# Kernel optimization log

Hardware: AMD Instinct MI355X
Metric: run time of the kernel (lower is better)

Reference implementation:

```python
import jax, jax.numpy as jnp
import numpy as np


def setup_inputs() -> dict:
    key = jax.random.key(0)
    k1, k2, k3 = jax.random.split(key, 3)
    preds = jax.random.normal(k1, (8, 3, 2048, 8), dtype=jnp.float32)
    gts = jax.random.normal(k2, (8, 3, 2048), dtype=jnp.float32)
    idx = jax.random.randint(k3, (64, 2), 0, 8, dtype=jnp.int64)
    return {"preds": preds, "gts": gts, "idx": idx}


def reference(preds, gts, idx):
    # preds: [bs, 3, N, seeds], gts: [bs, 3, N], idx: [num, 2] (batch, seed)
    num = idx.shape[0]
    # select (batch, seed) pairs -> [num, 3, N]
    p = jnp.transpose(preds, (0, 3, 1, 2))[idx[:, 0], idx[:, 1]]
    # gts expanded over seeds is constant in seed -> just index batch
    g = gts[idx[:, 0]]  # [num, 3, N]
    x = jnp.transpose(p, (0, 2, 1))  # [num, N, 3]
    y = jnp.transpose(g, (0, 2, 1))  # [num, N, 3]
    # P[b, i, j] = ||x_i||^2 + ||y_j||^2 - 2 x_i . y_j
    rx = jnp.sum(x * x, axis=-1)  # [num, N]
    ry = jnp.sum(y * y, axis=-1)  # [num, N]
    zz = jnp.einsum('bid,bjd->bij', x, y)  # [num, N, N]
    P = rx[:, :, None] + ry[:, None, :] - 2.0 * zz
    loss_1 = jnp.sum(jnp.min(P, axis=1))  # min over x for each y
    loss_2 = jnp.sum(jnp.min(P, axis=2))  # min over y for each x
    return (loss_1 + loss_2) / num
```

## Files before the change

### kernel.cpp

```cpp
#include <hip/hip_runtime.h>


#define NPTS 2048
#define NB 64
#define BLK 256

#define PREDS_A 49152
#define PREDS_C 16384
#define GTS_A 6144
#define GTS_C 2048

#define OFF_ROW   0
#define OFF_CPART 524288
#define OFF_PART  8912896
#define OFF_QPK   8916992
#define OFF_YPK   13111296
#define WS_REQ    17305600

using bf16x8  = __attribute__((ext_vector_type(8))) __bf16;
using short8v = __attribute__((ext_vector_type(8))) short;
using f32x16  = __attribute__((ext_vector_type(16))) float;

static __device__ __forceinline__ unsigned short f2bf(float f) {
    unsigned u = __float_as_uint(f);
    u = u + 0x7FFFu + ((u >> 16) & 1u);
    return (unsigned short)(u >> 16);
}
static __device__ __forceinline__ float bf2f(unsigned short h) {
    return __uint_as_float(((unsigned)h) << 16);
}
static __device__ __forceinline__ float min3f(float a, float b, float c) {
    return fminf(fminf(a, b), c);
}
static __device__ __forceinline__ float ctree(f32x16 a) {
    const float c0 = min3f(a[0], a[1], a[2]);
    const float c1 = min3f(a[3], a[4], a[5]);
    const float c2 = min3f(a[6], a[7], a[8]);
    const float c3 = min3f(a[9], a[10], a[11]);
    const float c4 = min3f(a[12], a[13], a[14]);
    const float d0 = min3f(c0, c1, a[15]);
    const float d1 = min3f(c2, c3, c4);
    return fminf(d0, d1);
}

__global__ __launch_bounds__(256) void cf_pack2(
    const float* __restrict__ preds, const float* __restrict__ gts,
    const int* __restrict__ idx,
    unsigned short* __restrict__ qpk, unsigned short* __restrict__ ypk)
{
    const int blk = blockIdx.x, tid = threadIdx.x;
    const unsigned short one = 0x3F80;
    if (blk < 512) {
        const int p = blk * 256 + tid;
        const int b = p >> 11, i = p & 2047;
        const int i0 = idx[2 * b], m1 = idx[2 * b + 1];
        const float* pb = preds + i0 * PREDS_A + m1 + i * 8;
        const float x0 = pb[0], x1 = pb[PREDS_C], x2 = pb[2 * PREDS_C];
        const float rx = fmaf(x0, x0, fmaf(x1, x1, x2 * x2));
        const float a0 = -2.f * x0, a1 = -2.f * x1, a2 = -2.f * x2;
        const unsigned short h0 = f2bf(a0), h1 = f2bf(a1), h2 = f2bf(a2);
        const unsigned short l0 = f2bf(a0 - bf2f(h0));
        const unsigned short l1 = f2bf(a1 - bf2f(h1));
        const unsigned short l2 = f2bf(a2 - bf2f(h2));
        const unsigned short rh = f2bf(rx), rl = f2bf(rx - bf2f(rh));
        alignas(16) unsigned short t[16] =
            {h0, h1, h2, h0, h1, h2, l0, l1, l2, rh, rl, one, one, 0, 0, 0};
        uint4* dst = (uint4*)(qpk + (size_t)p * 16);
        dst[0] = *(const uint4*)&t[0];
        dst[1] = *(const uint4*)&t[8];
    } else {
        const int p = (blk - 512) * 256 + tid;
        const int b = p >> 11, j = p & 2047;
        const int i0 = idx[2 * b];
        const float* gb = gts + i0 * GTS_A + j;
        const float y0 = gb[0], y1 = gb[GTS_C], y2 = gb[2 * GTS_C];
        const float ry = fmaf(y0, y0, fmaf(y1, y1, y2 * y2));
        const unsigned short h0 = f2bf(y0), h1 = f2bf(y1), h2 = f2bf(y2);
        const unsigned short l0 = f2bf(y0 - bf2f(h0));
        const unsigned short l1 = f2bf(y1 - bf2f(h1));
        const unsigned short l2 = f2bf(y2 - bf2f(h2));
        const unsigned short rh = f2bf(ry), rl = f2bf(ry - bf2f(rh));
        alignas(16) unsigned short t[16] =
            {h0, h1, h2, l0, l1, l2, h0, h1, h2, one, one, rh, rl, 0, 0, 0};
        uint4* dst = (uint4*)(ypk + (size_t)p * 16);
        dst[0] = *(const uint4*)&t[0];
        dst[1] = *(const uint4*)&t[8];
    }
}

__global__ __launch_bounds__(BLK, 4) void cf_mf3c(
    const unsigned short* __restrict__ qpk, const unsigned short* __restrict__ ypk,
    float* __restrict__ rowbuf, float* __restrict__ colpart)
{
    const int tid = threadIdx.x;
    const int bid = blockIdx.x;
    const int strip = bid & 15;
    const int b = bid >> 4;

    __shared__ float scolw[4][NPTS];

    const int l = tid & 63, w = tid >> 6;
    const int lc = l & 31, lh = l >> 5;

    const short8v* qv = (const short8v*)qpk;
    const short8v* yv = (const short8v*)ypk;

    const int arow = b * NPTS + strip * 128 + w * 32 + lc;
    const bf16x8 afrag = __builtin_bit_cast(bf16x8, qv[arow * 2 + lh]);

    float rm[16];
#pragma unroll
    for (int r = 0; r < 16; ++r) rm[r] = INFINITY;

    const f32x16 z = {0.f, 0.f, 0.f, 0.f, 0.f, 0.f, 0.f, 0.f,
                      0.f, 0.f, 0.f, 0.f, 0.f, 0.f, 0.f, 0.f};

    const short8v* yp = yv + (b * NPTS * 2 + lc * 2 + lh);

    bf16x8 curA = __builtin_bit_cast(bf16x8, yp[0]);
    bf16x8 curB = __builtin_bit_cast(bf16x8, yp[64]);

#pragma unroll 2
    for (int s = 0; s < 32; ++s) {
        const int nidx = (s < 31) ? (2 * s + 2) * 64 : 0;
        const bf16x8 nxtA = __builtin_bit_cast(bf16x8, yp[nidx]);
        const bf16x8 nxtB = __builtin_bit_cast(bf16x8, yp[nidx + 64]);

        __builtin_amdgcn_s_setprio(1);
        f32x16 accA = __builtin_amdgcn_mfma_f32_32x32x16_bf16(afrag, curA, z, 0, 0, 0);
        f32x16 accB = __builtin_amdgcn_mfma_f32_32x32x16_bf16(afrag, curB, z, 0, 0, 0);
        __builtin_amdgcn_s_setprio(0);

#pragma unroll
        for (int r = 0; r < 16; ++r) rm[r] = min3f(accA[r], accB[r], rm[r]);
        float cmA = ctree(accA);
        float cmB = ctree(accB);
        cmA = fminf(cmA, __shfl_xor(cmA, 32, 64));
        cmB = fminf(cmB, __shfl_xor(cmB, 32, 64));
        scolw[w][(2 * s) * 32 + lc] = cmA;
        scolw[w][(2 * s + 1) * 32 + lc] = cmB;

        curA = nxtA; curB = nxtB;
    }

#pragma unroll
    for (int r = 0; r < 16; ++r) {
        float v = rm[r];
        v = fminf(v, __shfl_xor(v, 1, 32));
        v = fminf(v, __shfl_xor(v, 2, 32));
        v = fminf(v, __shfl_xor(v, 4, 32));
        v = fminf(v, __shfl_xor(v, 8, 32));
        v = fminf(v, __shfl_xor(v, 16, 32));
        rm[r] = v;
    }
    if (lc == 0) {
        const int rbase = b * NPTS + strip * 128 + w * 32 + 4 * lh;
#pragma unroll
        for (int r = 0; r < 16; ++r)
            rowbuf[rbase + (r & 3) + 8 * (r >> 2)] = fmaxf(rm[r], 0.f);
    }

    __syncthreads();
    float* cp = colpart + (size_t)strip * (NB * NPTS) + b * NPTS;
    for (int k = tid; k < NPTS; k += BLK) {
        const float m = fminf(fminf(scolw[0][k], scolw[1][k]),
                              fminf(scolw[2][k], scolw[3][k]));
        cp[k] = fmaxf(m, 0.f);
    }
}

__global__ __launch_bounds__(256) void cf_reduce1n(
    const float* __restrict__ rowbuf, const float* __restrict__ colpart,
    float* __restrict__ partial)
{
    __shared__ float sm[4];
    const int blk = blockIdx.x, tid = threadIdx.x;
    float s = 0.0f;
    if (blk < 128) {
        const int base = blk * 1024;
        for (int i = 0; i < 4; ++i)
            s += rowbuf[base + tid + i * 256];
    } else {
        const int base = (blk - 128) * 1024;
        for (int i = 0; i < 4; ++i) {
            const int g = base + tid + i * 256;
            float m = INFINITY;
#pragma unroll
            for (int st = 0; st < 16; ++st)
                m = fminf(m, colpart[(size_t)st * (NB * NPTS) + g]);
            s += m;
        }
    }
#pragma unroll
    for (int off = 32; off > 0; off >>= 1)
        s += __shfl_down(s, off, 64);
    if ((tid & 63) == 0) sm[tid >> 6] = s;
    __syncthreads();
    if (tid == 0)
        partial[blk] = sm[0] + sm[1] + sm[2] + sm[3];
}

__global__ __launch_bounds__(256) void cf_reduce2n(const float* __restrict__ partial,
                                                   float* __restrict__ out) {
    __shared__ float sm[4];
    float s = partial[threadIdx.x];
#pragma unroll
    for (int off = 32; off > 0; off >>= 1)
        s += __shfl_down(s, off, 64);
    if ((threadIdx.x & 63) == 0) sm[threadIdx.x >> 6] = s;
    __syncthreads();
    if (threadIdx.x == 0)
        out[0] = (sm[0] + sm[1] + sm[2] + sm[3]) * (1.0f / 64.0f);
}

#define NMIN (2 * NB * NPTS)
#define FIT 128
#define FJT 128
#define PADI(j) ((j) + ((j) >> 4))

__global__ __launch_bounds__(256) void cf_init(unsigned* __restrict__ colbuf) {
    int i = blockIdx.x * 256 + threadIdx.x;
    colbuf[i] = 0x7F800000u;
}

__global__ __launch_bounds__(BLK, 4) void cf_tile_lds(
    const float* __restrict__ preds, const float* __restrict__ gts,
    const int* __restrict__ idx, unsigned* __restrict__ minbuf)
{
    const int tid = threadIdx.x;
    const int bid = blockIdx.x;
    const int it = bid & 15;
    const int b = bid >> 4;
    const int i0 = idx[2 * b];
    const int m1 = idx[2 * b + 1];
    const float* pbase = preds + i0 * PREDS_A + m1;
    const float* gbase = gts + i0 * GTS_A;

    __shared__ float4 sq[PADI(FIT - 1) + 2];
    __shared__ float4 sr[PADI(NPTS - 1) + 2];
    __shared__ float  scolw[4][FJT];

    if (tid < FIT) {
        const int i = it * FIT + tid;
        const float q0 = pbase[i * 8];
        const float q1 = pbase[i * 8 + PREDS_C];
        const float q2 = pbase[i * 8 + 2 * PREDS_C];
        const float rq = fmaf(q0, q0, fmaf(q1, q1, q2 * q2));
        sq[PADI(tid)] = make_float4(-2.f * q0, -2.f * q1, -2.f * q2, rq);
    }
#pragma unroll
    for (int k = 0; k < 8; ++k) {
        const int j = tid + BLK * k;
        const float r0 = gbase[j];
        const float r1 = gbase[j + GTS_C];
        const float r2 = gbase[j + 2 * GTS_C];
        const float rr = fmaf(r0, r0, fmaf(r1, r1, r2 * r2));
        sr[PADI(j)] = make_float4(r0, r1, r2, rr);
    }
    __syncthreads();

    const int ty = tid >> 4, tx = tid & 15;
    float nq0[8], nq1[8], nq2[8], rq[8], rmin[8];
#pragma unroll
    for (int u = 0; u < 8; ++u) {
        const float4 q = sq[PADI(ty * 8 + u)];
        nq0[u] = q.x; nq1[u] = q.y; nq2[u] = q.z; rq[u] = q.w;
        rmin[u] = INFINITY;
    }
    unsigned* rowbuf = minbuf;
    unsigned* colbuf = minbuf + NB * NPTS;

    for (int jt = 0; jt < NPTS / FJT; ++jt) {
        float4 r[8];
        const int rb = PADI(jt * FJT + tx * 8);
#pragma unroll
        for (int v = 0; v < 8; ++v) r[v] = sr[rb + v];
        float cmin[8];
#pragma unroll
        for (int v = 0; v < 8; ++v) cmin[v] = INFINITY;
#pragma unroll
        for (int v = 0; v < 8; v += 2) {
#pragma unroll
            for (int u = 0; u < 8; u += 2) {
                float s00 = fmaf(nq2[u], r[v].z, r[v].w);
                s00 = fmaf(nq1[u], r[v].y, s00);
                s00 = fmaf(nq0[u], r[v].x, s00);
                float s01 = fmaf(nq2[u], r[v + 1].z, r[v + 1].w);
                s01 = fmaf(nq1[u], r[v + 1].y, s01);
                s01 = fmaf(nq0[u], r[v + 1].x, s01);
                float s10 = fmaf(nq2[u + 1], r[v].z, r[v].w);
                s10 = fmaf(nq1[u + 1], r[v].y, s10);
                s10 = fmaf(nq0[u + 1], r[v].x, s10);
                float s11 = fmaf(nq2[u + 1], r[v + 1].z, r[v + 1].w);
                s11 = fmaf(nq1[u + 1], r[v + 1].y, s11);
                s11 = fmaf(nq0[u + 1], r[v + 1].x, s11);
                rmin[u]     = min3f(s00, s01, rmin[u]);
                rmin[u + 1] = min3f(s10, s11, rmin[u + 1]);
                const float d00 = s00 + rq[u];
                const float d10 = s10 + rq[u + 1];
                const float d01 = s01 + rq[u];
                const float d11 = s11 + rq[u + 1];
                cmin[v]     = min3f(d00, d10, cmin[v]);
                cmin[v + 1] = min3f(d01, d11, cmin[v + 1]);
            }
        }
#pragma unroll
        for (int v = 0; v < 8; ++v) {
            float c = cmin[v];
            c = fminf(c, __shfl_xor(c, 16, 64));
            c = fminf(c, __shfl_xor(c, 32, 64));
            cmin[v] = c;
        }
        if (((tid >> 4) & 3) == 0) {
            const int w = tid >> 6;
            *(float4*)&scolw[w][tx * 8]     = make_float4(cmin[0], cmin[1], cmin[2], cmin[3]);
            *(float4*)&scolw[w][tx * 8 + 4] = make_float4(cmin[4], cmin[5], cmin[6], cmin[7]);
        }
        __syncthreads();
        if (tid < FJT) {
            float m = fminf(min3f(scolw[0][tid], scolw[1][tid], scolw[2][tid]), scolw[3][tid]);
            m = fmaxf(m, 0.0f);
            atomicMin(&colbuf[b * NPTS + jt * FJT + tid], __float_as_uint(m));
        }
        __syncthreads();
    }
#pragma unroll
    for (int u = 0; u < 8; ++u) {
        float rm = rmin[u];
        rm = fminf(rm, __shfl_xor(rm, 1, 16));
        rm = fminf(rm, __shfl_xor(rm, 2, 16));
        rm = fminf(rm, __shfl_xor(rm, 4, 16));
        rm = fminf(rm, __shfl_xor(rm, 8, 16));
        rmin[u] = rm;
    }
    if (tx == 0) {
#pragma unroll
        for (int u = 0; u < 8; ++u) {
            const float d = fmaxf(rmin[u] + rq[u], 0.0f);
            rowbuf[b * NPTS + it * FIT + ty * 8 + u] = __float_as_uint(d);
        }
    }
}

__global__ __launch_bounds__(256) void cf_reduce1(const unsigned* __restrict__ minbuf,
                                                  float* __restrict__ partial) {
    __shared__ float sm[4];
    const int base = blockIdx.x * 1024;
    float s = 0.0f;
    for (int k = threadIdx.x; k < 1024; k += 256)
        s += __uint_as_float(minbuf[base + k]);
#pragma unroll
    for (int off = 32; off > 0; off >>= 1)
        s += __shfl_down(s, off, 64);
    if ((threadIdx.x & 63) == 0) sm[threadIdx.x >> 6] = s;
    __syncthreads();
    if (threadIdx.x == 0)
        partial[blockIdx.x] = sm[0] + sm[1] + sm[2] + sm[3];
}

__global__ __launch_bounds__(256) void cf_reduce2(const float* __restrict__ partial,
                                                  float* __restrict__ out) {
    __shared__ float sm[4];
    float s = (threadIdx.x < 128) ? partial[threadIdx.x] : 0.f;
#pragma unroll
    for (int off = 32; off > 0; off >>= 1)
        s += __shfl_down(s, off, 64);
    if ((threadIdx.x & 63) == 0) sm[threadIdx.x >> 6] = s;
    __syncthreads();
    if (threadIdx.x == 0)
        out[0] = (sm[0] + sm[1] + sm[2] + sm[3]) * (1.0f / 64.0f);
}

extern "C" void kernel_launch(void* const* d_in, const int* in_sizes, int n_in,
                              void* d_out, int out_size, void* d_ws, size_t ws_size,
                              hipStream_t stream) {
    const float* preds = (const float*)d_in[0];
    const float* gts   = (const float*)d_in[1];
    const int*   idx   = (const int*)d_in[2];
    float* out = (float*)d_out;

    if (ws_size >= (size_t)WS_REQ) {
        float* rowbuf  = (float*)((char*)d_ws + OFF_ROW);
        float* colpart = (float*)((char*)d_ws + OFF_CPART);
        float* partial = (float*)((char*)d_ws + OFF_PART);
        unsigned short* qpk = (unsigned short*)((char*)d_ws + OFF_QPK);
        unsigned short* ypk = (unsigned short*)((char*)d_ws + OFF_YPK);
        cf_pack2<<<1024, 256, 0, stream>>>(preds, gts, idx, qpk, ypk);
        cf_mf3c<<<NB * 16, BLK, 0, stream>>>(qpk, ypk, rowbuf, colpart);
        cf_reduce1n<<<256, 256, 0, stream>>>(rowbuf, colpart, partial);
        cf_reduce2n<<<1, 256, 0, stream>>>(partial, out);
    } else {
        unsigned* minbuf = (unsigned*)d_ws;
        unsigned* colbuf = minbuf + NB * NPTS;
        float* partial   = (float*)((char*)d_ws + NMIN * 4);
        cf_init<<<(NB * NPTS) / 256, 256, 0, stream>>>(colbuf);
        cf_tile_lds<<<NB * (NPTS / FIT), BLK, 0, stream>>>(preds, gts, idx, minbuf);
        cf_reduce1<<<NMIN / 1024, 256, 0, stream>>>(minbuf, partial);
        cf_reduce2<<<1, 256, 0, stream>>>(partial, out);
    }
}
```

Before: 38.27 us.

## Split column range in half to double MFMA kernel grid size

The MFMA distance kernel now splits each strip's 2048 columns into two halves handled by separate blocks, doubling the grid from 1024 to 2048 blocks and halving per-block LDS. Row minima are written as two partial buffers and merged in the reduction kernel with an extra min. This targets low occupancy and tail imbalance on the many-CU GPU. The cost is extra rowpart writes and reads plus duplicated A-fragment loads.

Result: slower. 40.68 us (+6.3%).

```diff
diff --git a/kernel.cpp b/kernel.cpp
--- a/kernel.cpp
+++ b/kernel.cpp
@@ -11,11 +11,11 @@
 #define GTS_C 2048
 
 #define OFF_ROW   0
-#define OFF_CPART 524288
-#define OFF_PART  8912896
-#define OFF_QPK   8916992
-#define OFF_YPK   13111296
-#define WS_REQ    17305600
+#define OFF_CPART 1048576
+#define OFF_PART  9437184
+#define OFF_QPK   9441280
+#define OFF_YPK   13635584
+#define WS_REQ    17829888
 
 using bf16x8  = __attribute__((ext_vector_type(8))) __bf16;
 using short8v = __attribute__((ext_vector_type(8))) short;
@@ -88,16 +88,17 @@
     }
 }
 
-__global__ __launch_bounds__(BLK, 4) void cf_mf3c(
+__global__ __launch_bounds__(BLK, 4) void cf_mf3d(
     const unsigned short* __restrict__ qpk, const unsigned short* __restrict__ ypk,
-    float* __restrict__ rowbuf, float* __restrict__ colpart)
+    float* __restrict__ rowpart, float* __restrict__ colpart)
 {
     const int tid = threadIdx.x;
     const int bid = blockIdx.x;
-    const int strip = bid & 15;
-    const int b = bid >> 4;
-
-    __shared__ float scolw[4][NPTS];
+    const int colhalf = bid & 1;
+    const int strip = (bid >> 1) & 15;
+    const int b = bid >> 5;
+
+    __shared__ float scolw[4][1024];
 
     const int l = tid & 63, w = tid >> 6;
     const int lc = l & 31, lh = l >> 5;
@@ -115,14 +116,14 @@
     const f32x16 z = {0.f, 0.f, 0.f, 0.f, 0.f, 0.f, 0.f, 0.f,
                       0.f, 0.f, 0.f, 0.f, 0.f, 0.f, 0.f, 0.f};
 
-    const short8v* yp = yv + (b * NPTS * 2 + lc * 2 + lh);
+    const short8v* yp = yv + ((b * NPTS + colhalf * 1024) * 2 + lc * 2 + lh);
 
     bf16x8 curA = __builtin_bit_cast(bf16x8, yp[0]);
     bf16x8 curB = __builtin_bit_cast(bf16x8, yp[64]);
 
 #pragma unroll 2
-    for (int s = 0; s < 32; ++s) {
-        const int nidx = (s < 31) ? (2 * s + 2) * 64 : 0;
+    for (int s = 0; s < 16; ++s) {
+        const int nidx = (s < 15) ? (2 * s + 2) * 64 : 0;
         const bf16x8 nxtA = __builtin_bit_cast(bf16x8, yp[nidx]);
         const bf16x8 nxtB = __builtin_bit_cast(bf16x8, yp[nidx + 64]);
 
@@ -154,15 +155,15 @@
         rm[r] = v;
     }
     if (lc == 0) {
-        const int rbase = b * NPTS + strip * 128 + w * 32 + 4 * lh;
+        const int rbase = colhalf * (NB * NPTS) + b * NPTS + strip * 128 + w * 32 + 4 * lh;
 #pragma unroll
         for (int r = 0; r < 16; ++r)
-            rowbuf[rbase + (r & 3) + 8 * (r >> 2)] = fmaxf(rm[r], 0.f);
-    }
-
-    __syncthreads();
-    float* cp = colpart + (size_t)strip * (NB * NPTS) + b * NPTS;
-    for (int k = tid; k < NPTS; k += BLK) {
+            rowpart[rbase + (r & 3) + 8 * (r >> 2)] = fmaxf(rm[r], 0.f);
+    }
+
+    __syncthreads();
+    float* cp = colpart + (size_t)strip * (NB * NPTS) + b * NPTS + colhalf * 1024;
+    for (int k = tid; k < 1024; k += BLK) {
         const float m = fminf(fminf(scolw[0][k], scolw[1][k]),
                               fminf(scolw[2][k], scolw[3][k]));
         cp[k] = fmaxf(m, 0.f);
@@ -170,7 +171,7 @@
 }
 
 __global__ __launch_bounds__(256) void cf_reduce1n(
-    const float* __restrict__ rowbuf, const float* __restrict__ colpart,
+    const float* __restrict__ rowpart, const float* __restrict__ colpart,
     float* __restrict__ partial)
 {
     __shared__ float sm[4];
@@ -178,8 +179,10 @@
     float s = 0.0f;
     if (blk < 128) {
         const int base = blk * 1024;
-        for (int i = 0; i < 4; ++i)
-            s += rowbuf[base + tid + i * 256];
+        for (int i = 0; i < 4; ++i) {
+            const int g = base + tid + i * 256;
+            s += fminf(rowpart[g], rowpart[NB * NPTS + g]);
+        }
     } else {
         const int base = (blk - 128) * 1024;
         for (int i = 0; i < 4; ++i) {
@@ -380,14 +383,14 @@
     float* out = (float*)d_out;
 
     if (ws_size >= (size_t)WS_REQ) {
-        float* rowbuf  = (float*)((char*)d_ws + OFF_ROW);
+        float* rowpart = (float*)((char*)d_ws + OFF_ROW);
         float* colpart = (float*)((char*)d_ws + OFF_CPART);
         float* partial = (float*)((char*)d_ws + OFF_PART);
         unsigned short* qpk = (unsigned short*)((char*)d_ws + OFF_QPK);
         unsigned short* ypk = (unsigned short*)((char*)d_ws + OFF_YPK);
         cf_pack2<<<1024, 256, 0, stream>>>(preds, gts, idx, qpk, ypk);
-        cf_mf3c<<<NB * 16, BLK, 0, stream>>>(qpk, ypk, rowbuf, colpart);
-        cf_reduce1n<<<256, 256, 0, stream>>>(rowbuf, colpart, partial);
+        cf_mf3d<<<NB * 32, BLK, 0, stream>>>(qpk, ypk, rowpart, colpart);
+        cf_reduce1n<<<256, 256, 0, stream>>>(rowpart, colpart, partial);
         cf_reduce2n<<<1, 256, 0, stream>>>(partial, out);
     } else {
         unsigned* minbuf = (unsigned*)d_ws;
```

## Build A fragments in the MFMA kernel and merge column minima with atomicMin

Applied to the files above, without the earlier changes.

The pred-side bf16 hi/lo packing moves out of the pack kernel and into the MFMA kernel, which now reads preds directly and builds the A fragment in registers. That drops the qpk workspace round trip. The 16-strip column-partial buffer is replaced by a single colbuf that the prep kernel fills with +inf and each block merges into with atomicMin on the float bit pattern, which is valid because the values are clamped non-negative. This shrinks the reduce kernel's reads and the workspace, at the cost of atomic contention across 16 strips per batch and some extra per-thread conversion work.

Result: no change. 37.75 us (-1.4%).

```diff
diff --git a/kernel.cpp b/kernel.cpp
--- a/kernel.cpp
+++ b/kernel.cpp
@@ -11,11 +11,10 @@
 #define GTS_C 2048
 
 #define OFF_ROW   0
-#define OFF_CPART 524288
-#define OFF_PART  8912896
-#define OFF_QPK   8916992
-#define OFF_YPK   13111296
-#define WS_REQ    17305600
+#define OFF_COL   524288
+#define OFF_PART  1048576
+#define OFF_YPK   1052672
+#define WS_REQ    (OFF_YPK + NB * NPTS * 32)
 
 using bf16x8  = __attribute__((ext_vector_type(8))) __bf16;
 using short8v = __attribute__((ext_vector_type(8))) short;
@@ -43,32 +42,15 @@
     return fminf(d0, d1);
 }
 
-__global__ __launch_bounds__(256) void cf_pack2(
-    const float* __restrict__ preds, const float* __restrict__ gts,
-    const int* __restrict__ idx,
-    unsigned short* __restrict__ qpk, unsigned short* __restrict__ ypk)
+__global__ __launch_bounds__(256) void cf_prep(
+    const float* __restrict__ gts, const int* __restrict__ idx,
+    unsigned* __restrict__ colbuf, unsigned short* __restrict__ ypk)
 {
     const int blk = blockIdx.x, tid = threadIdx.x;
-    const unsigned short one = 0x3F80;
     if (blk < 512) {
-        const int p = blk * 256 + tid;
-        const int b = p >> 11, i = p & 2047;
-        const int i0 = idx[2 * b], m1 = idx[2 * b + 1];
-        const float* pb = preds + i0 * PREDS_A + m1 + i * 8;
-        const float x0 = pb[0], x1 = pb[PREDS_C], x2 = pb[2 * PREDS_C];
-        const float rx = fmaf(x0, x0, fmaf(x1, x1, x2 * x2));
-        const float a0 = -2.f * x0, a1 = -2.f * x1, a2 = -2.f * x2;
-        const unsigned short h0 = f2bf(a0), h1 = f2bf(a1), h2 = f2bf(a2);
-        const unsigned short l0 = f2bf(a0 - bf2f(h0));
-        const unsigned short l1 = f2bf(a1 - bf2f(h1));
-        const unsigned short l2 = f2bf(a2 - bf2f(h2));
-        const unsigned short rh = f2bf(rx), rl = f2bf(rx - bf2f(rh));
-        alignas(16) unsigned short t[16] =
-            {h0, h1, h2, h0, h1, h2, l0, l1, l2, rh, rl, one, one, 0, 0, 0};
-        uint4* dst = (uint4*)(qpk + (size_t)p * 16);
-        dst[0] = *(const uint4*)&t[0];
-        dst[1] = *(const uint4*)&t[8];
+        colbuf[blk * 256 + tid] = 0x7F800000u;
     } else {
+        const unsigned short one = 0x3F80;
         const int p = (blk - 512) * 256 + tid;
         const int b = p >> 11, j = p & 2047;
         const int i0 = idx[2 * b];
@@ -88,25 +70,43 @@
     }
 }
 
-__global__ __launch_bounds__(BLK, 4) void cf_mf3c(
-    const unsigned short* __restrict__ qpk, const unsigned short* __restrict__ ypk,
-    float* __restrict__ rowbuf, float* __restrict__ colpart)
+__global__ __launch_bounds__(BLK, 4) void cf_mf4(
+    const float* __restrict__ preds, const int* __restrict__ idx,
+    const unsigned short* __restrict__ ypk,
+    float* __restrict__ rowbuf, unsigned* __restrict__ colbuf)
 {
     const int tid = threadIdx.x;
-    const int bid = blockIdx.x;
-    const int strip = bid & 15;
-    const int b = bid >> 4;
+    const int strip = blockIdx.x & 15;
+    const int b = blockIdx.x >> 4;
 
     __shared__ float scolw[4][NPTS];
 
     const int l = tid & 63, w = tid >> 6;
     const int lc = l & 31, lh = l >> 5;
 
-    const short8v* qv = (const short8v*)qpk;
-    const short8v* yv = (const short8v*)ypk;
-
-    const int arow = b * NPTS + strip * 128 + w * 32 + lc;
-    const bf16x8 afrag = __builtin_bit_cast(bf16x8, qv[arow * 2 + lh]);
+    const int i0 = idx[2 * b], m1 = idx[2 * b + 1];
+    {
+    }
+    const float* pb = preds + i0 * PREDS_A + m1 + (strip * 128 + w * 32 + lc) * 8;
+    const float x0 = pb[0], x1 = pb[PREDS_C], x2 = pb[2 * PREDS_C];
+    const float rx = fmaf(x0, x0, fmaf(x1, x1, x2 * x2));
+    const float a0 = -2.f * x0, a1 = -2.f * x1, a2 = -2.f * x2;
+    const unsigned short h0 = f2bf(a0), h1 = f2bf(a1), h2 = f2bf(a2);
+    const unsigned short lo0 = f2bf(a0 - bf2f(h0));
+    const unsigned short lo1 = f2bf(a1 - bf2f(h1));
+    const unsigned short lo2 = f2bf(a2 - bf2f(h2));
+    const unsigned short rh = f2bf(rx), rl = f2bf(rx - bf2f(rh));
+    const unsigned short one = 0x3F80;
+    short8v av;
+    av[0] = (short)(lh ? lo2 : h0);
+    av[1] = (short)(lh ? rh  : h1);
+    av[2] = (short)(lh ? rl  : h2);
+    av[3] = (short)(lh ? one : h0);
+    av[4] = (short)(lh ? one : h1);
+    av[5] = (short)(lh ? (unsigned short)0 : h2);
+    av[6] = (short)(lh ? (unsigned short)0 : lo0);
+    av[7] = (short)(lh ? (unsigned short)0 : lo1);
+    const bf16x8 afrag = __builtin_bit_cast(bf16x8, av);
 
     float rm[16];
 #pragma unroll
@@ -115,7 +115,7 @@
     const f32x16 z = {0.f, 0.f, 0.f, 0.f, 0.f, 0.f, 0.f, 0.f,
                       0.f, 0.f, 0.f, 0.f, 0.f, 0.f, 0.f, 0.f};
 
-    const short8v* yp = yv + (b * NPTS * 2 + lc * 2 + lh);
+    const short8v* yp = (const short8v*)ypk + (b * NPTS * 2 + lc * 2 + lh);
 
     bf16x8 curA = __builtin_bit_cast(bf16x8, yp[0]);
     bf16x8 curB = __builtin_bit_cast(bf16x8, yp[64]);
@@ -161,49 +161,41 @@
     }
 
     __syncthreads();
-    float* cp = colpart + (size_t)strip * (NB * NPTS) + b * NPTS;
     for (int k = tid; k < NPTS; k += BLK) {
         const float m = fminf(fminf(scolw[0][k], scolw[1][k]),
                               fminf(scolw[2][k], scolw[3][k]));
-        cp[k] = fmaxf(m, 0.f);
-    }
-}
-
-__global__ __launch_bounds__(256) void cf_reduce1n(
-    const float* __restrict__ rowbuf, const float* __restrict__ colpart,
+        atomicMin(&colbuf[b * NPTS + k], __float_as_uint(fmaxf(m, 0.f)));
+    }
+}
+
+__global__ __launch_bounds__(256) void cf_red1(
+    const float* __restrict__ rowbuf, const unsigned* __restrict__ colbuf,
     float* __restrict__ partial)
 {
     __shared__ float sm[4];
     const int blk = blockIdx.x, tid = threadIdx.x;
     float s = 0.0f;
-    if (blk < 128) {
-        const int base = blk * 1024;
-        for (int i = 0; i < 4; ++i)
-            s += rowbuf[base + tid + i * 256];
+    if (blk < 64) {
+        const float* rp = rowbuf + blk * 2048;
+#pragma unroll
+        for (int i = 0; i < 8; ++i) s += rp[tid + i * 256];
     } else {
-        const int base = (blk - 128) * 1024;
-        for (int i = 0; i < 4; ++i) {
-            const int g = base + tid + i * 256;
-            float m = INFINITY;
-#pragma unroll
-            for (int st = 0; st < 16; ++st)
-                m = fminf(m, colpart[(size_t)st * (NB * NPTS) + g]);
-            s += m;
-        }
+        const unsigned* cp = colbuf + (blk - 64) * 2048;
+#pragma unroll
+        for (int i = 0; i < 8; ++i) s += __uint_as_float(cp[tid + i * 256]);
     }
 #pragma unroll
     for (int off = 32; off > 0; off >>= 1)
         s += __shfl_down(s, off, 64);
     if ((tid & 63) == 0) sm[tid >> 6] = s;
     __syncthreads();
-    if (tid == 0)
-        partial[blk] = sm[0] + sm[1] + sm[2] + sm[3];
-}
-
-__global__ __launch_bounds__(256) void cf_reduce2n(const float* __restrict__ partial,
-                                                   float* __restrict__ out) {
+    if (tid == 0) partial[blk] = sm[0] + sm[1] + sm[2] + sm[3];
+}
+
+__global__ __launch_bounds__(256) void cf_red2(const float* __restrict__ partial,
+                                               float* __restrict__ out) {
     __shared__ float sm[4];
-    float s = partial[threadIdx.x];
+    float s = (threadIdx.x < 128) ? partial[threadIdx.x] : 0.f;
 #pragma unroll
     for (int off = 32; off > 0; off >>= 1)
         s += __shfl_down(s, off, 64);
@@ -380,15 +372,14 @@
     float* out = (float*)d_out;
 
     if (ws_size >= (size_t)WS_REQ) {
-        float* rowbuf  = (float*)((char*)d_ws + OFF_ROW);
-        float* colpart = (float*)((char*)d_ws + OFF_CPART);
-        float* partial = (float*)((char*)d_ws + OFF_PART);
-        unsigned short* qpk = (unsigned short*)((char*)d_ws + OFF_QPK);
+        float*    rowbuf  = (float*)((char*)d_ws + OFF_ROW);
+        unsigned* colbuf  = (unsigned*)((char*)d_ws + OFF_COL);
+        float*    partial = (float*)((char*)d_ws + OFF_PART);
         unsigned short* ypk = (unsigned short*)((char*)d_ws + OFF_YPK);
-        cf_pack2<<<1024, 256, 0, stream>>>(preds, gts, idx, qpk, ypk);
-        cf_mf3c<<<NB * 16, BLK, 0, stream>>>(qpk, ypk, rowbuf, colpart);
-        cf_reduce1n<<<256, 256, 0, stream>>>(rowbuf, colpart, partial);
-        cf_reduce2n<<<1, 256, 0, stream>>>(partial, out);
+        cf_prep<<<1024, 256, 0, stream>>>(gts, idx, colbuf, ypk);
+        cf_mf4<<<NB * 16, BLK, 0, stream>>>(preds, idx, ypk, rowbuf, colbuf);
+        cf_red1<<<128, 256, 0, stream>>>(rowbuf, colbuf, partial);
+        cf_red2<<<1, 256, 0, stream>>>(partial, out);
     } else {
         unsigned* minbuf = (unsigned*)d_ws;
         unsigned* colbuf = minbuf + NB * NPTS;
```
